# Optimization experiments

Measured on AMD Instinct MI355X. Metric: run time of the kernel, lower is better.

Reference implementation:

```python
import jax, jax.numpy as jnp
import numpy as np

KS = 7
DIM = 1024
HEADS = 16
B = 2048

def _rpb_index(ks):
    # Replicates the torch buffer: relative_position_index, shape [ks*ks, ks*ks]
    ch = np.arange(ks)
    coords = np.stack(np.meshgrid(ch, ch, indexing='ij')).reshape(2, -1)  # [2, N]
    rel = coords[:, :, None] - coords[:, None, :]                          # [2, N, N]
    rel = rel.transpose(1, 2, 0).copy()                                    # [N, N, 2]
    rel[:, :, 0] += ks - 1
    rel[:, :, 1] += ks - 1
    rel[:, :, 0] *= 2 * ks - 1
    idx = np.flipud(np.fliplr(rel.sum(-1)))
    return jnp.asarray(idx.copy())

def setup_inputs() -> dict:
    key = jax.random.key(0)
    ks = jax.random.split(key, 4)
    x = jax.random.normal(ks[0], (B, KS, KS, DIM), dtype=jnp.float32)
    qkv_w = jax.random.normal(ks[1], (3 * DIM, DIM), dtype=jnp.float32) * (DIM ** -0.5)
    qkv_b = jnp.zeros((3 * DIM,), dtype=jnp.float32)
    rpb = jax.random.normal(ks[2], (HEADS, 2 * KS - 1, 2 * KS - 1), dtype=jnp.float32) * 0.02
    proj_w = jax.random.normal(ks[3], (DIM, DIM), dtype=jnp.float32) * (DIM ** -0.5)
    proj_b = jnp.zeros((DIM,), dtype=jnp.float32)
    return {"x": x, "qkv_w": qkv_w, "qkv_b": qkv_b, "rpb": rpb, "proj_w": proj_w, "proj_b": proj_b}

def reference(x, qkv_w, qkv_b, rpb, proj_w, proj_b):
    Bn, H, W, C = x.shape
    ksz = H
    N = H * W
    heads = rpb.shape[0]
    hd = C // heads
    scale = hd ** -0.5
    idx = _rpb_index(ksz)  # [N, N] int

    qkv = x.reshape(Bn, N, C) @ qkv_w.T + qkv_b              # [B, N, 3C]
    qkv = qkv.reshape(Bn, N, 3, heads, hd).transpose(2, 0, 3, 1, 4)  # [3, B, h, N, hd]
    q, k, v = qkv[0] * scale, qkv[1], qkv[2]

    attn = jnp.einsum('bhnd,bhmd->bhnm', q, k)               # [B, h, N, N]
    # gather relative-position bias: rpb[h, 2k-1, 2k-1] -> flat [(2k-1)^2, h] -> [N, N, h]
    bias = rpb.transpose(1, 2, 0).reshape(-1, heads)[idx.reshape(-1)]
    bias = bias.reshape(N, N, heads).transpose(2, 0, 1)      # [h, N, N]
    attn = jax.nn.softmax(attn + bias[None], axis=-1)

    out = jnp.einsum('bhnm,bhmd->bhnd', attn, v)             # [B, h, N, hd]
    out = out.transpose(0, 2, 1, 3).reshape(Bn, H, W, C)
    return out @ proj_w.T + proj_b
```

## Files before the change

### kernel.cpp

```cpp
#include <hip/hip_runtime.h>


typedef _Float16 f16;
typedef _Float16 f16x8 __attribute__((ext_vector_type(8)));
typedef _Float16 f16x4 __attribute__((ext_vector_type(4)));
typedef float f32x4 __attribute__((ext_vector_type(4)));

#define G1P(p) ((const __attribute__((address_space(1))) unsigned int*)(p))
#define L3P(p) ((__attribute__((address_space(3))) unsigned int*)(p))

static const size_t MROW_MAX = 100351;

__global__ void cvt_kernel(const float* __restrict__ in, f16* __restrict__ out, int n4) {
  int i = blockIdx.x * blockDim.x + threadIdx.x;
  int stride = gridDim.x * blockDim.x;
  const float4* in4 = (const float4*)in;
  f16x4* out4 = (f16x4*)out;
  for (; i < n4; i += stride) {
    float4 v = in4[i];
    f16x4 o = { (f16)v.x, (f16)v.y, (f16)v.z, (f16)v.w };
    out4[i] = o;
  }
}

__global__ void bias_kernel(const float* __restrict__ rpb, f16* __restrict__ bias_t) {
  int h = blockIdx.x;
  for (int e = threadIdx.x; e < 4096; e += blockDim.x) {
    int m = e >> 6, n = e & 63;
    float v = -60000.f;
    if (n < 49 && m < 49) {
      int in_ = n / 7, jn = n % 7, im = m / 7, jm = m % 7;
      v = rpb[h * 169 + (im - in_ + 6) * 13 + (jm - jn + 6)] * 1.44269504f;
    }
    bias_t[h * 4096 + e] = (f16)v;
  }
}

#define VM4 asm volatile("s_waitcnt vmcnt(4)" ::: "memory")
#define VM0 asm volatile("s_waitcnt vmcnt(0)" ::: "memory")
#define NOVM ((void)0)
#define NOSTG ((void)0)

#define STAGE(GB, ROW0, COL0, LDSOFF)                                              \
  {                                                                                \
    const f16* s0_ = (GB) + (size_t)((ROW0) + wid * 32 + srow) * K + ((COL0) + sce); \
    __builtin_amdgcn_global_load_lds(G1P(s0_), L3P(lds + (LDSOFF) + wid * 2048), 16, 0, 0); \
    const f16* s1_ = s0_ + (size_t)16 * K;                                         \
    __builtin_amdgcn_global_load_lds(G1P(s1_), L3P(lds + (LDSOFF) + wid * 2048 + 1024), 16, 0, 0); \
  }

#define MFMA4(AREG, ROW)                                                           \
  acc[ROW][0] = __builtin_amdgcn_mfma_f32_16x16x32_f16(AREG, b0, acc[ROW][0], 0, 0, 0); \
  acc[ROW][1] = __builtin_amdgcn_mfma_f32_16x16x32_f16(AREG, b1, acc[ROW][1], 0, 0, 0); \
  acc[ROW][2] = __builtin_amdgcn_mfma_f32_16x16x32_f16(AREG, b2, acc[ROW][2], 0, 0, 0); \
  acc[ROW][3] = __builtin_amdgcn_mfma_f32_16x16x32_f16(AREG, b3, acc[ROW][3], 0, 0, 0);

#define PHASE(ABASE, BBASE, MH, STG, VMW)                                          \
  {                                                                                \
    f16x8 a0 = *(const f16x8*)((ABASE) + (wm * 128 + (MH) * 64 +  0 + l15) * 64 + swz); \
    f16x8 a1 = *(const f16x8*)((ABASE) + (wm * 128 + (MH) * 64 + 16 + l15) * 64 + swz); \
    f16x8 a2 = *(const f16x8*)((ABASE) + (wm * 128 + (MH) * 64 + 32 + l15) * 64 + swz); \
    f16x8 a3 = *(const f16x8*)((ABASE) + (wm * 128 + (MH) * 64 + 48 + l15) * 64 + swz); \
    if ((MH) == 0) {                                                               \
      b0 = *(const f16x8*)((BBASE) + (wn * 64 +  0 + l15) * 64 + swz);             \
      b1 = *(const f16x8*)((BBASE) + (wn * 64 + 16 + l15) * 64 + swz);             \
      b2 = *(const f16x8*)((BBASE) + (wn * 64 + 32 + l15) * 64 + swz);             \
      b3 = *(const f16x8*)((BBASE) + (wn * 64 + 48 + l15) * 64 + swz);             \
    }                                                                              \
    STG;                                                                           \
    __builtin_amdgcn_s_barrier();                                                  \
    asm volatile("s_waitcnt lgkmcnt(0)" ::: "memory");                             \
    __builtin_amdgcn_sched_barrier(0);                                             \
    __builtin_amdgcn_s_setprio(1);                                                 \
    MFMA4(a0, (MH) * 4 + 0) MFMA4(a1, (MH) * 4 + 1)                                \
    MFMA4(a2, (MH) * 4 + 2) MFMA4(a3, (MH) * 4 + 3)                                \
    __builtin_amdgcn_s_setprio(0);                                                 \
    VMW;                                                                           \
    __builtin_amdgcn_s_barrier();                                                  \
  }

template <typename OutT>
__global__ __launch_bounds__(512, 2)
void gemm256(const f16* __restrict__ A, const f16* __restrict__ B,
             const float* __restrict__ bias, OutT* __restrict__ C,
             int N, int K, int ntiles_n) {
  __shared__ char lds[131072];
  const int tid = threadIdx.x;
  const int wid = tid >> 6, ln = tid & 63;
  const int l15 = ln & 15, lhi = ln >> 4;
  const int wm = wid >> 2, wn = wid & 3;
  const int srow = ln >> 2;
  const int sce = (((ln & 3) ^ ((ln >> 3) & 3)) << 3);
  const int swz = ((lhi ^ ((l15 >> 1) & 3)) << 4);

  const int nblk = gridDim.x;
  const int wg = (blockIdx.x & 7) * (nblk >> 3) + (blockIdx.x >> 3);
  const int bn = wg % ntiles_n, bm = wg / ntiles_n;
  const int m0 = bm * 256, n0 = bn * 256;

  f32x4 acc[8][4];
#pragma unroll
  for (int i = 0; i < 8; ++i)
#pragma unroll
    for (int j = 0; j < 4; ++j) acc[i][j] = (f32x4){0.f, 0.f, 0.f, 0.f};
  f16x8 b0, b1, b2, b3;

  STAGE(A, m0, 0, 0);
  STAGE(B, n0, 0, 32768);
  STAGE(A, m0, 32, 16384);
  STAGE(B, n0, 32, 49152);
  STAGE(A, m0, 64, 65536);
  STAGE(B, n0, 64, 98304);
  VM4;
  __builtin_amdgcn_s_barrier();

  for (int i = 0; i < 7; ++i) {
    const int cT1k1 = (2 * i + 1) * 64 + 32;
    const int cT2k0 = (2 * i + 2) * 64;
    const int cT2k1 = cT2k0 + 32;
    const int cT3k0 = (2 * i + 3) * 64;
    PHASE(lds + 0,      lds + 32768,  0, STAGE(A, m0, cT1k1, 81920),  NOVM);
    PHASE(lds + 0,      lds + 32768,  1, STAGE(B, n0, cT1k1, 114688), NOVM);
    PHASE(lds + 16384,  lds + 49152,  0, STAGE(A, m0, cT2k0, 0),      NOVM);
    PHASE(lds + 16384,  lds + 49152,  1, STAGE(B, n0, cT2k0, 32768),  VM4);
    PHASE(lds + 65536,  lds + 98304,  0, STAGE(A, m0, cT2k1, 16384),  NOVM);
    PHASE(lds + 65536,  lds + 98304,  1, STAGE(B, n0, cT2k1, 49152),  NOVM);
    PHASE(lds + 81920,  lds + 114688, 0, STAGE(A, m0, cT3k0, 65536),  NOVM);
    PHASE(lds + 81920,  lds + 114688, 1, STAGE(B, n0, cT3k0, 98304),  VM4);
  }
  PHASE(lds + 0,      lds + 32768,  0, STAGE(A, m0, 15 * 64 + 32, 81920),  NOVM);
  PHASE(lds + 0,      lds + 32768,  1, STAGE(B, n0, 15 * 64 + 32, 114688), NOVM);
  PHASE(lds + 16384,  lds + 49152,  0, NOSTG, NOVM);
  PHASE(lds + 16384,  lds + 49152,  1, NOSTG, VM0);
  PHASE(lds + 65536,  lds + 98304,  0, NOSTG, NOVM);
  PHASE(lds + 65536,  lds + 98304,  1, NOSTG, NOVM);
  PHASE(lds + 81920,  lds + 114688, 0, NOSTG, NOVM);
  PHASE(lds + 81920,  lds + 114688, 1, NOSTG, NOVM);

  float bv[4];
#pragma unroll
  for (int j = 0; j < 4; ++j) bv[j] = bias[n0 + wn * 64 + j * 16 + l15];
#pragma unroll
  for (int ii = 0; ii < 8; ++ii)
#pragma unroll
    for (int j = 0; j < 4; ++j)
#pragma unroll
      for (int r = 0; r < 4; ++r) {
        int gr = m0 + wm * 128 + ii * 16 + lhi * 4 + r;
        int gc = n0 + wn * 64 + j * 16 + l15;
        C[(size_t)gr * N + gc] = (OutT)(acc[ii][j][r] + bv[j]);
      }
}

__global__ __launch_bounds__(64)
void attn_kernel(const f16* __restrict__ qkv,
                 const f16* __restrict__ bias_t,
                 f16* __restrict__ out) {
  __shared__ char lds[16384];
  const int bh = blockIdx.x;
  const int b = bh >> 4, h = bh & 15;
  const int ln = threadIdx.x;
  const int l15 = ln & 15, lhi = ln >> 4;
  const size_t base = (size_t)b * 49;

  {
    int rA = ln >> 3, lc = ln & 7;
#pragma unroll
    for (int c = 0; c < 8; ++c) {
      int r = c * 8 + rA;
      int ce = (lc ^ (r & 7)) << 3;
      size_t row = base + r;
      if (row > MROW_MAX) row = MROW_MAX;
      const f16* g = qkv + row * 3072 + 1024 + h * 64 + ce;
      __builtin_amdgcn_global_load_lds(G1P(g), L3P(lds + c * 1024), 16, 0, 0);
    }
  }

  size_t rowv = base + ln;
  if (rowv > MROW_MAX) rowv = MROW_MAX;
  const f16* vp = qkv + rowv * 3072 + 2048 + h * 64;
  f16x8 vr[8];
#pragma unroll
  for (int j = 0; j < 8; ++j) vr[j] = *(const f16x8*)(vp + j * 8);

  f16x8 qf[4][2];
#pragma unroll
  for (int t = 0; t < 4; ++t) {
    size_t row = base + t * 16 + l15;
    if (row > MROW_MAX) row = MROW_MAX;
    const f16* qp = qkv + row * 3072 + h * 64 + lhi * 8;
    qf[t][0] = *(const f16x8*)(qp);
    qf[t][1] = *(const f16x8*)(qp + 32);
  }

  const f16* bb = bias_t + h * 4096;
  f16x4 bq[4][4];
#pragma unroll
  for (int i = 0; i < 4; ++i)
#pragma unroll
    for (int j = 0; j < 4; ++j)
      bq[i][j] = *(const f16x4*)(bb + (j * 16 + l15) * 64 + i * 16 + lhi * 4);

#pragma unroll
  for (int d = 0; d < 64; ++d)
    *(f16*)(lds + 8192 + d * 128 + ((ln * 2) ^ ((d & 7) << 4))) = vr[d >> 3][d & 7];

  asm volatile("s_waitcnt vmcnt(0)" ::: "memory");
  __builtin_amdgcn_sched_barrier(0);

  f32x4 acc[4][4];
#pragma unroll
  for (int i = 0; i < 4; ++i)
#pragma unroll
    for (int j = 0; j < 4; ++j) acc[i][j] = (f32x4){0.f, 0.f, 0.f, 0.f};
#pragma unroll
  for (int kk = 0; kk < 2; ++kk) {
    f16x8 bf[4];
#pragma unroll
    for (int t = 0; t < 4; ++t) {
      int mr = t * 16 + l15;
      int pb = (kk * 64 + lhi * 16) ^ ((mr & 7) << 4);
      bf[t] = *(const f16x8*)(lds + mr * 128 + pb);
    }
    __builtin_amdgcn_s_setprio(1);
#pragma unroll
    for (int i = 0; i < 4; ++i)
#pragma unroll
      for (int j = 0; j < 4; ++j)
        acc[i][j] = __builtin_amdgcn_mfma_f32_16x16x32_f16(qf[i][kk], bf[j], acc[i][j], 0, 0, 0);
    __builtin_amdgcn_s_setprio(0);
  }

  const float SC = 0.125f * 1.44269504f;
#pragma unroll
  for (int i = 0; i < 4; ++i) {
#pragma unroll
    for (int r = 0; r < 4; ++r) {
      int n = i * 16 + lhi * 4 + r;
      float lv[4];
#pragma unroll
      for (int j = 0; j < 4; ++j)
        lv[j] = acc[i][j][r] * SC + (float)bq[i][j][r];
      float Mx = fmaxf(fmaxf(lv[0], lv[1]), fmaxf(lv[2], lv[3]));
#pragma unroll
      for (int off = 1; off < 16; off <<= 1) Mx = fmaxf(Mx, __shfl_xor(Mx, off));
      float s = 0.f;
#pragma unroll
      for (int j = 0; j < 4; ++j) { lv[j] = exp2f(lv[j] - Mx); s += lv[j]; }
#pragma unroll
      for (int off = 1; off < 16; off <<= 1) s += __shfl_xor(s, off);
      float inv = 1.f / s;
#pragma unroll
      for (int j = 0; j < 4; ++j) {
        int m = j * 16 + l15;
        *(f16*)(lds + n * 128 + ((m * 2) ^ ((n & 7) << 4))) = (f16)(lv[j] * inv);
      }
    }
  }

  f32x4 o[4][4];
#pragma unroll
  for (int i = 0; i < 4; ++i)
#pragma unroll
    for (int j = 0; j < 4; ++j) o[i][j] = (f32x4){0.f, 0.f, 0.f, 0.f};
#pragma unroll
  for (int kk = 0; kk < 2; ++kk) {
    f16x8 af[4], bf[4];
#pragma unroll
    for (int t = 0; t < 4; ++t) {
      int nr = t * 16 + l15;
      int pb = (kk * 64 + lhi * 16) ^ ((nr & 7) << 4);
      af[t] = *(const f16x8*)(lds + nr * 128 + pb);
      bf[t] = *(const f16x8*)(lds + 8192 + nr * 128 + pb);
    }
    __builtin_amdgcn_s_setprio(1);
#pragma unroll
    for (int i = 0; i < 4; ++i)
#pragma unroll
      for (int j = 0; j < 4; ++j)
        o[i][j] = __builtin_amdgcn_mfma_f32_16x16x32_f16(af[i], bf[j], o[i][j], 0, 0, 0);
    __builtin_amdgcn_s_setprio(0);
  }
#pragma unroll
  for (int i = 0; i < 4; ++i)
#pragma unroll
    for (int j = 0; j < 4; ++j)
#pragma unroll
      for (int r = 0; r < 4; ++r) {
        int n = i * 16 + lhi * 4 + r;
        if (n < 49)
          out[(base + n) * 1024 + h * 64 + j * 16 + l15] = (f16)o[i][j][r];
      }
}

extern "C" void kernel_launch(void* const* d_in, const int* in_sizes, int n_in,
                              void* d_out, int out_size, void* d_ws, size_t ws_size,
                              hipStream_t stream) {
  const float* x      = (const float*)d_in[0];
  const float* qkv_w  = (const float*)d_in[1];
  const float* qkv_b  = (const float*)d_in[2];
  const float* rpb    = (const float*)d_in[3];
  const float* proj_w = (const float*)d_in[4];
  const float* proj_b = (const float*)d_in[5];
  float* out = (float*)d_out;

  char* ws = (char*)d_ws;
  f16*   x16      = (f16*)(ws);
  f16*   wq16     = (f16*)(ws + 205520896);
  f16*   wp16     = (f16*)(ws + 211812352);
  f16*   qkv16    = (f16*)(ws + 213909504);
  f16*   attn16   = (f16*)(ws + 830472192);
  f16*   bias_t   = (f16*)(ws + 1035993088);

  cvt_kernel<<<2048, 256, 0, stream>>>(x, x16, 102760448 / 4);
  cvt_kernel<<<1024, 256, 0, stream>>>(qkv_w, wq16, 3145728 / 4);
  cvt_kernel<<<512, 256, 0, stream>>>(proj_w, wp16, 1048576 / 4);
  bias_kernel<<<16, 64, 0, stream>>>(rpb, bias_t);

  gemm256<f16><<<4704, 512, 0, stream>>>(x16, wq16, qkv_b, qkv16, 3072, 1024, 12);
  attn_kernel<<<2048 * 16, 64, 0, stream>>>(qkv16, bias_t, attn16);
  gemm256<float><<<1568, 512, 0, stream>>>(attn16, wp16, proj_b, out, 1024, 1024, 4);
}
```

Before: 1.321 ms.

## Compute transposed scores in registers and shuffle probabilities directly into PV operands

The attention kernel now computes S^T = K·Q^T with K and Q fragments loaded straight into registers, so each lane holds a full key column per query. Softmax reductions shrink to two cross-lane shuffles, and the probabilities are packed to f16 and redistributed with shuffles into A-operand layout instead of going through LDS. LDS drops to 8KB, holding V only, and launch bounds request 4 blocks per SM to raise occupancy. The bias table is transposed to match. The cost is more register pressure and extra shuffle instructions, which could limit the occupancy gain.

```diff
diff --git a/kernel.cpp b/kernel.cpp
--- a/kernel.cpp
+++ b/kernel.cpp
@@ -26,7 +26,7 @@
 __global__ void bias_kernel(const float* __restrict__ rpb, f16* __restrict__ bias_t) {
   int h = blockIdx.x;
   for (int e = threadIdx.x; e < 4096; e += blockDim.x) {
-    int m = e >> 6, n = e & 63;
+    int n = e >> 6, m = e & 63;
     float v = -60000.f;
     if (n < 49 && m < 49) {
       int in_ = n / 7, jn = n % 7, im = m / 7, jm = m % 7;
@@ -152,133 +152,133 @@
       }
 }
 
-__global__ __launch_bounds__(64)
+__global__ __launch_bounds__(64, 4)
 void attn_kernel(const f16* __restrict__ qkv,
                  const f16* __restrict__ bias_t,
                  f16* __restrict__ out) {
-  __shared__ char lds[16384];
+  __shared__ char lds[8192];
   const int bh = blockIdx.x;
   const int b = bh >> 4, h = bh & 15;
   const int ln = threadIdx.x;
   const int l15 = ln & 15, lhi = ln >> 4;
   const size_t base = (size_t)b * 49;
 
-  {
-    int rA = ln >> 3, lc = ln & 7;
-#pragma unroll
-    for (int c = 0; c < 8; ++c) {
-      int r = c * 8 + rA;
-      int ce = (lc ^ (r & 7)) << 3;
-      size_t row = base + r;
-      if (row > MROW_MAX) row = MROW_MAX;
-      const f16* g = qkv + row * 3072 + 1024 + h * 64 + ce;
-      __builtin_amdgcn_global_load_lds(G1P(g), L3P(lds + c * 1024), 16, 0, 0);
-    }
-  }
-
+  f16x8 kf[4][2];
+#pragma unroll
+  for (int t = 0; t < 4; ++t) {
+    size_t row = base + t * 16 + l15;
+    if (row > MROW_MAX) row = MROW_MAX;
+    const f16* kp = qkv + row * 3072 + 1024 + h * 64 + lhi * 8;
+    kf[t][0] = *(const f16x8*)(kp);
+    kf[t][1] = *(const f16x8*)(kp + 32);
+  }
+  f16x8 qb[4][2];
+#pragma unroll
+  for (int u = 0; u < 4; ++u) {
+    size_t row = base + u * 16 + l15;
+    if (row > MROW_MAX) row = MROW_MAX;
+    const f16* qp = qkv + row * 3072 + h * 64 + lhi * 8;
+    qb[u][0] = *(const f16x8*)(qp);
+    qb[u][1] = *(const f16x8*)(qp + 32);
+  }
   size_t rowv = base + ln;
   if (rowv > MROW_MAX) rowv = MROW_MAX;
   const f16* vp = qkv + rowv * 3072 + 2048 + h * 64;
   f16x8 vr[8];
 #pragma unroll
   for (int j = 0; j < 8; ++j) vr[j] = *(const f16x8*)(vp + j * 8);
-
-  f16x8 qf[4][2];
-#pragma unroll
-  for (int t = 0; t < 4; ++t) {
-    size_t row = base + t * 16 + l15;
-    if (row > MROW_MAX) row = MROW_MAX;
-    const f16* qp = qkv + row * 3072 + h * 64 + lhi * 8;
-    qf[t][0] = *(const f16x8*)(qp);
-    qf[t][1] = *(const f16x8*)(qp + 32);
-  }
-
   const f16* bb = bias_t + h * 4096;
   f16x4 bq[4][4];
 #pragma unroll
+  for (int u = 0; u < 4; ++u)
+#pragma unroll
+    for (int t = 0; t < 4; ++t)
+      bq[u][t] = *(const f16x4*)(bb + (u * 16 + l15) * 64 + t * 16 + lhi * 4);
+
+#pragma unroll
+  for (int d = 0; d < 64; ++d)
+    *(f16*)(lds + d * 128 + ((ln * 2) ^ ((d & 7) << 4))) = vr[d >> 3][d & 7];
+
+  const float SC = 0.125f * 1.44269504f;
+  const int s0 = ((lhi & 1) * 2) * 16 + l15;
+  const int s1 = s0 + 16;
+  const bool hi = (lhi >> 1) & 1;
+  int afr[4][2][4];
+#pragma unroll
+  for (int u = 0; u < 4; ++u) {
+    f32x4 acc[4];
+#pragma unroll
+    for (int t = 0; t < 4; ++t) acc[t] = (f32x4){0.f, 0.f, 0.f, 0.f};
+#pragma unroll
+    for (int kk = 0; kk < 2; ++kk) {
+      __builtin_amdgcn_s_setprio(1);
+#pragma unroll
+      for (int t = 0; t < 4; ++t)
+        acc[t] = __builtin_amdgcn_mfma_f32_16x16x32_f16(kf[t][kk], qb[u][kk], acc[t], 0, 0, 0);
+      __builtin_amdgcn_s_setprio(0);
+    }
+    float lv[4][4];
+#pragma unroll
+    for (int t = 0; t < 4; ++t)
+#pragma unroll
+      for (int r = 0; r < 4; ++r)
+        lv[t][r] = acc[t][r] * SC + (float)bq[u][t][r];
+    float Mx = lv[0][0];
+#pragma unroll
+    for (int t = 0; t < 4; ++t)
+#pragma unroll
+      for (int r = 0; r < 4; ++r) Mx = fmaxf(Mx, lv[t][r]);
+    Mx = fmaxf(Mx, __shfl_xor(Mx, 16));
+    Mx = fmaxf(Mx, __shfl_xor(Mx, 32));
+    float s = 0.f;
+#pragma unroll
+    for (int t = 0; t < 4; ++t)
+#pragma unroll
+      for (int r = 0; r < 4; ++r) { lv[t][r] = exp2f(lv[t][r] - Mx); s += lv[t][r]; }
+    s += __shfl_xor(s, 16);
+    s += __shfl_xor(s, 32);
+    float inv = 1.f / s;
+    int pk[4][2];
+#pragma unroll
+    for (int t = 0; t < 4; ++t)
+#pragma unroll
+      for (int pp = 0; pp < 2; ++pp)
+        pk[t][pp] = __builtin_bit_cast(int,
+            __builtin_amdgcn_cvt_pkrtz(lv[t][2 * pp] * inv, lv[t][2 * pp + 1] * inv));
+#pragma unroll
+    for (int kk = 0; kk < 2; ++kk)
+#pragma unroll
+      for (int j = 0; j < 4; ++j) {
+        int src = (j >> 1) ? s1 : s0;
+        int a0 = __shfl(pk[kk * 2][j & 1], src);
+        int a1 = __shfl(pk[kk * 2 + 1][j & 1], src);
+        afr[u][kk][j] = hi ? a1 : a0;
+      }
+  }
+
+  f32x4 o[4][4];
+#pragma unroll
   for (int i = 0; i < 4; ++i)
 #pragma unroll
-    for (int j = 0; j < 4; ++j)
-      bq[i][j] = *(const f16x4*)(bb + (j * 16 + l15) * 64 + i * 16 + lhi * 4);
-
-#pragma unroll
-  for (int d = 0; d < 64; ++d)
-    *(f16*)(lds + 8192 + d * 128 + ((ln * 2) ^ ((d & 7) << 4))) = vr[d >> 3][d & 7];
-
-  asm volatile("s_waitcnt vmcnt(0)" ::: "memory");
-  __builtin_amdgcn_sched_barrier(0);
-
-  f32x4 acc[4][4];
-#pragma unroll
-  for (int i = 0; i < 4; ++i)
-#pragma unroll
-    for (int j = 0; j < 4; ++j) acc[i][j] = (f32x4){0.f, 0.f, 0.f, 0.f};
+    for (int j = 0; j < 4; ++j) o[i][j] = (f32x4){0.f, 0.f, 0.f, 0.f};
 #pragma unroll
   for (int kk = 0; kk < 2; ++kk) {
     f16x8 bf[4];
 #pragma unroll
-    for (int t = 0; t < 4; ++t) {
-      int mr = t * 16 + l15;
-      int pb = (kk * 64 + lhi * 16) ^ ((mr & 7) << 4);
-      bf[t] = *(const f16x8*)(lds + mr * 128 + pb);
+    for (int j = 0; j < 4; ++j) {
+      int dr = j * 16 + l15;
+      bf[j] = *(const f16x8*)(lds + dr * 128 + ((kk * 64 + lhi * 16) ^ ((dr & 7) << 4)));
     }
     __builtin_amdgcn_s_setprio(1);
 #pragma unroll
-    for (int i = 0; i < 4; ++i)
+    for (int i = 0; i < 4; ++i) {
+      union { int w[4]; f16x8 v; } au;
+#pragma unroll
+      for (int j = 0; j < 4; ++j) au.w[j] = afr[i][kk][j];
 #pragma unroll
       for (int j = 0; j < 4; ++j)
-        acc[i][j] = __builtin_amdgcn_mfma_f32_16x16x32_f16(qf[i][kk], bf[j], acc[i][j], 0, 0, 0);
-    __builtin_amdgcn_s_setprio(0);
-  }
-
-  const float SC = 0.125f * 1.44269504f;
-#pragma unroll
-  for (int i = 0; i < 4; ++i) {
-#pragma unroll
-    for (int r = 0; r < 4; ++r) {
-      int n = i * 16 + lhi * 4 + r;
-      float lv[4];
-#pragma unroll
-      for (int j = 0; j < 4; ++j)
-        lv[j] = acc[i][j][r] * SC + (float)bq[i][j][r];
-      float Mx = fmaxf(fmaxf(lv[0], lv[1]), fmaxf(lv[2], lv[3]));
-#pragma unroll
-      for (int off = 1; off < 16; off <<= 1) Mx = fmaxf(Mx, __shfl_xor(Mx, off));
-      float s = 0.f;
-#pragma unroll
-      for (int j = 0; j < 4; ++j) { lv[j] = exp2f(lv[j] - Mx); s += lv[j]; }
-#pragma unroll
-      for (int off = 1; off < 16; off <<= 1) s += __shfl_xor(s, off);
-      float inv = 1.f / s;
-#pragma unroll
-      for (int j = 0; j < 4; ++j) {
-        int m = j * 16 + l15;
-        *(f16*)(lds + n * 128 + ((m * 2) ^ ((n & 7) << 4))) = (f16)(lv[j] * inv);
-      }
+        o[i][j] = __builtin_amdgcn_mfma_f32_16x16x32_f16(au.v, bf[j], o[i][j], 0, 0, 0);
     }
-  }
-
-  f32x4 o[4][4];
-#pragma unroll
-  for (int i = 0; i < 4; ++i)
-#pragma unroll
-    for (int j = 0; j < 4; ++j) o[i][j] = (f32x4){0.f, 0.f, 0.f, 0.f};
-#pragma unroll
-  for (int kk = 0; kk < 2; ++kk) {
-    f16x8 af[4], bf[4];
-#pragma unroll
-    for (int t = 0; t < 4; ++t) {
-      int nr = t * 16 + l15;
-      int pb = (kk * 64 + lhi * 16) ^ ((nr & 7) << 4);
-      af[t] = *(const f16x8*)(lds + nr * 128 + pb);
-      bf[t] = *(const f16x8*)(lds + 8192 + nr * 128 + pb);
-    }
-    __builtin_amdgcn_s_setprio(1);
-#pragma unroll
-    for (int i = 0; i < 4; ++i)
-#pragma unroll
-      for (int j = 0; j < 4; ++j)
-        o[i][j] = __builtin_amdgcn_mfma_f32_16x16x32_f16(af[i], bf[j], o[i][j], 0, 0, 0);
     __builtin_amdgcn_s_setprio(0);
   }
 #pragma unroll
```

Result: slower. 1.397 ms (+5.8%).

## Write QKV GEMM output in per-(batch,head) contiguous layout for attention

Applied to the files above, without the earlier changes.

The QKV GEMM epilogue now scatters each output element into a [batch, head, q/k/v, token, dim] layout, so each attention block reads its Q, K and V as contiguous 3136-element slabs. Before, those reads were strided rows of 3072 halfs. The attention kernel's address math is simplified to match, with row clamping done inside the slab. The goal is better locality for the attention loads, at the cost of an integer divide per row and less coalesced 2-byte stores in the GEMM epilogue.

```diff
diff --git a/kernel.cpp b/kernel.cpp
--- a/kernel.cpp
+++ b/kernel.cpp
@@ -8,8 +8,6 @@
 
 #define G1P(p) ((const __attribute__((address_space(1))) unsigned int*)(p))
 #define L3P(p) ((__attribute__((address_space(3))) unsigned int*)(p))
-
-static const size_t MROW_MAX = 100351;
 
 __global__ void cvt_kernel(const float* __restrict__ in, f16* __restrict__ out, int n4) {
   int i = blockIdx.x * blockDim.x + threadIdx.x;
@@ -79,7 +77,7 @@
     __builtin_amdgcn_s_barrier();                                                  \
   }
 
-template <typename OutT>
+template <typename OutT, bool HB>
 __global__ __launch_bounds__(512, 2)
 void gemm256(const f16* __restrict__ A, const f16* __restrict__ B,
              const float* __restrict__ bias, OutT* __restrict__ C,
@@ -143,13 +141,26 @@
 #pragma unroll
   for (int ii = 0; ii < 8; ++ii)
 #pragma unroll
-    for (int j = 0; j < 4; ++j)
-#pragma unroll
-      for (int r = 0; r < 4; ++r) {
-        int gr = m0 + wm * 128 + ii * 16 + lhi * 4 + r;
-        int gc = n0 + wn * 64 + j * 16 + l15;
-        C[(size_t)gr * N + gc] = (OutT)(acc[ii][j][r] + bv[j]);
+    for (int r = 0; r < 4; ++r) {
+      int gr = m0 + wm * 128 + ii * 16 + lhi * 4 + r;
+      if (HB) {
+        int bw = gr / 49, n = gr - bw * 49;
+#pragma unroll
+        for (int j = 0; j < 4; ++j) {
+          int gc = n0 + wn * 64 + j * 16 + l15;
+          int which = gc >> 10, rem = gc & 1023;
+          int h = rem >> 6, d = rem & 63;
+          size_t addr = (((size_t)bw * 16 + h) * 3 + which) * 3136 + n * 64 + d;
+          C[addr] = (OutT)(acc[ii][j][r] + bv[j]);
+        }
+      } else {
+#pragma unroll
+        for (int j = 0; j < 4; ++j) {
+          int gc = n0 + wn * 64 + j * 16 + l15;
+          C[(size_t)gr * N + gc] = (OutT)(acc[ii][j][r] + bv[j]);
+        }
       }
+    }
 }
 
 __global__ __launch_bounds__(64)
@@ -162,23 +173,24 @@
   const int ln = threadIdx.x;
   const int l15 = ln & 15, lhi = ln >> 4;
   const size_t base = (size_t)b * 49;
+  const size_t qb = (size_t)bh * 3 * 3136;
+  const size_t kb = qb + 3136;
+  const size_t vb = qb + 6272;
 
   {
     int rA = ln >> 3, lc = ln & 7;
 #pragma unroll
     for (int c = 0; c < 8; ++c) {
       int r = c * 8 + rA;
+      int rc = r > 48 ? 48 : r;
       int ce = (lc ^ (r & 7)) << 3;
-      size_t row = base + r;
-      if (row > MROW_MAX) row = MROW_MAX;
-      const f16* g = qkv + row * 3072 + 1024 + h * 64 + ce;
+      const f16* g = qkv + kb + rc * 64 + ce;
       __builtin_amdgcn_global_load_lds(G1P(g), L3P(lds + c * 1024), 16, 0, 0);
     }
   }
 
-  size_t rowv = base + ln;
-  if (rowv > MROW_MAX) rowv = MROW_MAX;
-  const f16* vp = qkv + rowv * 3072 + 2048 + h * 64;
+  int rv = ln > 48 ? 48 : ln;
+  const f16* vp = qkv + vb + rv * 64;
   f16x8 vr[8];
 #pragma unroll
   for (int j = 0; j < 8; ++j) vr[j] = *(const f16x8*)(vp + j * 8);
@@ -186,9 +198,9 @@
   f16x8 qf[4][2];
 #pragma unroll
   for (int t = 0; t < 4; ++t) {
-    size_t row = base + t * 16 + l15;
-    if (row > MROW_MAX) row = MROW_MAX;
-    const f16* qp = qkv + row * 3072 + h * 64 + lhi * 8;
+    int rq = t * 16 + l15;
+    if (rq > 48) rq = 48;
+    const f16* qp = qkv + qb + rq * 64 + lhi * 8;
     qf[t][0] = *(const f16x8*)(qp);
     qf[t][1] = *(const f16x8*)(qp + 32);
   }
@@ -317,7 +329,7 @@
   cvt_kernel<<<512, 256, 0, stream>>>(proj_w, wp16, 1048576 / 4);
   bias_kernel<<<16, 64, 0, stream>>>(rpb, bias_t);
 
-  gemm256<f16><<<4704, 512, 0, stream>>>(x16, wq16, qkv_b, qkv16, 3072, 1024, 12);
+  gemm256<f16, true><<<4704, 512, 0, stream>>>(x16, wq16, qkv_b, qkv16, 3072, 1024, 12);
   attn_kernel<<<2048 * 16, 64, 0, stream>>>(qkv16, bias_t, attn16);
-  gemm256<float><<<1568, 512, 0, stream>>>(attn16, wp16, proj_b, out, 1024, 1024, 4);
-}
+  gemm256<float, false><<<1568, 512, 0, stream>>>(attn16, wp16, proj_b, out, 1024, 1024, 4);
+}
```

New measurement: 1.252 ms. -5.2%, faster.
